# Performance work log

Measured on AMD Instinct MI355X. Metric: run time of the kernel, lower is better.

Reference implementation:

```python
import jax, jax.numpy as jnp
import numpy as np
from jax import lax

VOCAB, EMB, HID = 32000, 512, 1024
T, B = 256, 16


def setup_inputs() -> dict:
    key = jax.random.key(0)
    k1, k2, k3, k4, k5, k6 = jax.random.split(key, 6)
    s = lambda fan_in: 1.0 / np.sqrt(fan_in)
    return {
        "x": jax.random.randint(k1, (T, B), 0, VOCAB),
        "h": jnp.zeros((B, HID), jnp.float32),
        "emb": jax.random.normal(k2, (VOCAB, EMB), jnp.float32),
        "Wz": jax.random.normal(k3, (HID, EMB + HID), jnp.float32) * s(EMB + HID),
        "Wr": jax.random.normal(k4, (HID, EMB + HID), jnp.float32) * s(EMB + HID),
        "W": jax.random.normal(k5, (HID, EMB + HID), jnp.float32) * s(EMB + HID),
        "Wd": jax.random.normal(k6, (VOCAB, HID), jnp.float32) * s(HID),
    }


def reference(x, h, emb, Wz, Wr, W, Wd):
    x_emb = emb[x]  # [T, B, EMB]

    def step(h_prev, xe):
        y = jnp.concatenate([h_prev, xe], axis=1)           # [B, HID+EMB]
        z = jax.nn.sigmoid(y @ Wz.T)                        # [B, HID]
        r = jax.nn.sigmoid(y @ Wr.T)                        # [B, HID]
        cand = jnp.tanh(jnp.concatenate([r * h_prev, xe], axis=1) @ W.T)
        h_new = (1.0 - z) * h_prev + z * cand
        return h_new, h_new

    _, all_h = lax.scan(step, h, x_emb)                     # [T, B, HID]
    all_y = jnp.einsum('tbh,vh->tbv', all_h, Wd)            # [T, B, VOCAB]
    return all_h, all_y
```

## Files before the change

kernel.cpp:

```cpp
#include <hip/hip_runtime.h>


using bf16x8 = __attribute__((ext_vector_type(8))) __bf16;
using f32x4  = __attribute__((ext_vector_type(4))) float;

#define GRUB 64
#define TOTB 256
#define NTILE 250
#define NGRP  32

__device__ __forceinline__ unsigned short f2bf(float f) {
  unsigned u = __builtin_bit_cast(unsigned, f);
  u += 0x7FFFu + ((u >> 16) & 1u);
  return (unsigned short)(u >> 16);
}

__device__ __forceinline__ f32x4 mfma16(bf16x8 a, bf16x8 b, f32x4 c) {
  return __builtin_amdgcn_mfma_f32_16x16x32_bf16(a, b, c, 0, 0, 0);
}

__device__ __forceinline__ void ust32(unsigned* p, unsigned v) {
  __hip_atomic_store(p, v, __ATOMIC_RELAXED, __HIP_MEMORY_SCOPE_AGENT);
}
__device__ __forceinline__ unsigned uld32(const unsigned* p) {
  return __hip_atomic_load(p, __ATOMIC_RELAXED, __HIP_MEMORY_SCOPE_AGENT);
}


__global__ void prep_w(const float* __restrict__ Wz, const float* __restrict__ Wr,
                       const float* __restrict__ Wm,
                       unsigned short* __restrict__ Whall,
                       unsigned short* __restrict__ Wxall) {
  int i = blockIdx.x * 256 + threadIdx.x;
  int g   = i / 393216;
  int rem = i % 393216;
  int j   = rem / 384;
  int k   = (rem % 384) * 4;
  const float* src = (g == 0) ? Wz : (g == 1) ? Wr : Wm;
  float4 v = *(const float4*)(src + (size_t)j * 1536 + k);
  ushort4 o;
  o.x = f2bf(v.x); o.y = f2bf(v.y); o.z = f2bf(v.z); o.w = f2bf(v.w);
  if (k < 1024)
    *(ushort4*)(Whall + ((size_t)(g * 1024 + j) * 1024 + k)) = o;
  else
    *(ushort4*)(Wxall + ((size_t)(g * 1024 + j) * 512 + (k - 1024))) = o;
}

__global__ void prep_wd(const float* __restrict__ Wd, unsigned short* __restrict__ Wdbf) {
  size_t i = (size_t)blockIdx.x * 256 + threadIdx.x;
  float4 v = *(const float4*)(Wd + i * 4);
  ushort4 o;
  o.x = f2bf(v.x); o.y = f2bf(v.y); o.z = f2bf(v.z); o.w = f2bf(v.w);
  *(ushort4*)(Wdbf + i * 4) = o;
}

__global__ void prep_xe(const int* __restrict__ x, const float* __restrict__ emb,
                        unsigned short* __restrict__ xebf) {
  int i  = blockIdx.x * 256 + threadIdx.x;
  int tb = i >> 7, k = (i & 127) * 4;
  int tok = x[tb];
  float4 v = *(const float4*)(emb + (size_t)tok * 512 + k);
  ushort4 o;
  o.x = f2bf(v.x); o.y = f2bf(v.y); o.z = f2bf(v.z); o.w = f2bf(v.w);
  *(ushort4*)(xebf + (size_t)tb * 512 + k) = o;
}

__global__ void prep_h(const float* __restrict__ h, unsigned short* __restrict__ hbf) {
  int i = blockIdx.x * 256 + threadIdx.x;
  hbf[i] = f2bf(h[i]);
}

__global__ __launch_bounds__(256) void gemm_bt(
    const unsigned short* __restrict__ A, const unsigned short* __restrict__ B,
    float* __restrict__ C, int M, int N, int K, int lda, int ldb, int ldc) {
  __shared__ uint4 As[128 * 5];
  __shared__ uint4 Bs[128 * 5];
  const int tid  = threadIdx.x;
  const int wid  = tid >> 6, lane = tid & 63;
  const int wr   = wid >> 1, wc = wid & 1;
  const int m0   = blockIdx.x * 128, n0 = blockIdx.y * 128;
  const int lr   = lane & 15, lk = lane >> 4;

  f32x4 acc[4][4] = {};
  const int nk = K >> 5;
  for (int kt = 0; kt < nk; ++kt) {
#pragma unroll
    for (int c = 0; c < 2; ++c) {
      int chunk = c * 256 + tid;
      int row = chunk >> 2, kc = chunk & 3;
      As[row * 5 + kc] = *(const uint4*)(A + (size_t)(m0 + row) * lda + kt * 32 + kc * 8);
      Bs[row * 5 + kc] = *(const uint4*)(B + (size_t)(n0 + row) * ldb + kt * 32 + kc * 8);
    }
    __syncthreads();
    bf16x8 af[4], bg[4];
#pragma unroll
    for (int i = 0; i < 4; ++i) {
      af[i] = __builtin_bit_cast(bf16x8, As[(wr * 64 + i * 16 + lr) * 5 + lk]);
      bg[i] = __builtin_bit_cast(bf16x8, Bs[(wc * 64 + i * 16 + lr) * 5 + lk]);
    }
#pragma unroll
    for (int i = 0; i < 4; ++i)
#pragma unroll
      for (int j = 0; j < 4; ++j)
        acc[i][j] = mfma16(af[i], bg[j], acc[i][j]);
    __syncthreads();
  }
#pragma unroll
  for (int i = 0; i < 4; ++i) {
    int mb = m0 + wr * 64 + i * 16 + lk * 4;
#pragma unroll
    for (int j = 0; j < 4; ++j) {
      int n = n0 + wc * 64 + j * 16 + lr;
#pragma unroll
      for (int q = 0; q < 4; ++q)
        C[(size_t)(mb + q) * ldc + n] = acc[i][j][q];
    }
  }
}


__device__ __forceinline__ void flag_bar(unsigned* flags, unsigned seq) {
  __syncthreads();
  if (threadIdx.x < 64) {
    if (threadIdx.x == 0)
      ust32(&flags[blockIdx.x * 32], seq);
    unsigned* f = &flags[threadIdx.x * 32];
    while (uld32(f) < seq) {}
  }
  __syncthreads();
}

__global__ __launch_bounds__(256, 1) void mega(
    const unsigned short* __restrict__ Whall, const float* __restrict__ Gx,
    const unsigned short* __restrict__ h0bf, const float* __restrict__ h0f,
    unsigned short* __restrict__ rhs, float* __restrict__ outh,
    unsigned short* __restrict__ allh,
    const unsigned short* __restrict__ Wdbf, float* __restrict__ outy,
    unsigned* __restrict__ flags) {
  __shared__ uint4 smem[6672];
  const int tid = threadIdx.x;
  const int bid = blockIdx.x;
  unsigned* stepp = flags + 2048;
  unsigned* ctrp  = flags + 2080;

  if (bid < GRUB) {
    uint4* Wl = smem;
    float (*red)[4][16][16] = (float (*)[4][16][16])(smem + 6144);
    const int lane = tid & 63, wq = tid >> 6;
    const int c0   = bid * 16;
    const int lr   = lane & 15, lk = lane >> 4;
    const int bKu  = wq * 32;

    for (int it = 0; it < 24; ++it) {
      int chunk = it * 256 + tid;
      int g = chunk >> 11, rem = chunk & 2047;
      int cl = rem >> 7, k8 = rem & 127;
      uint4 v = *(const uint4*)(Whall + ((size_t)(g * 1024 + c0 + cl) * 1024 + k8 * 8));
      Wl[(g * 16 + cl) * 128 + (k8 ^ (cl & 7))] = v;
    }

    const int b_  = tid >> 4, cl_ = tid & 15;
    const int cg  = c0 + cl_;
    float hp = h0f[b_ * 1024 + cg];
    float zv = 0.f;
    __syncthreads();

    for (int t = 0; t < 256; ++t) {
      const size_t tb = (size_t)t * 16 + b_;
      float gz = Gx[tb * 3072 + cg];
      float gr = Gx[tb * 3072 + 1024 + cg];
      float gc = Gx[tb * 3072 + 2048 + cg];

      const uint4* hp4 = (t == 0) ? (const uint4*)h0bf
                                  : (const uint4*)(allh + (size_t)(t - 1) * 16384);
      f32x4 az = {}, ar = {};
#pragma unroll
      for (int kk = 0; kk < 8; ++kk) {
        int ku = bKu + kk * 4 + lk;
        bf16x8 a  = __builtin_bit_cast(bf16x8, hp4[lr * 128 + ku]);
        bf16x8 bz = __builtin_bit_cast(bf16x8, Wl[(0 * 16 + lr) * 128 + (ku ^ (lr & 7))]);
        bf16x8 br = __builtin_bit_cast(bf16x8, Wl[(1 * 16 + lr) * 128 + (ku ^ (lr & 7))]);
        az = mfma16(a, bz, az);
        ar = mfma16(a, br, ar);
      }
#pragma unroll
      for (int q = 0; q < 4; ++q) {
        red[0][wq][lk * 4 + q][lr] = az[q];
        red[1][wq][lk * 4 + q][lr] = ar[q];
      }
      __syncthreads();
      {
        float sz = red[0][0][b_][cl_] + red[0][1][b_][cl_] + red[0][2][b_][cl_] +
                   red[0][3][b_][cl_] + gz;
        float sr = red[1][0][b_][cl_] + red[1][1][b_][cl_] + red[1][2][b_][cl_] +
                   red[1][3][b_][cl_] + gr;
        zv = 1.f / (1.f + __expf(-sz));
        float rv = 1.f / (1.f + __expf(-sr));
        unsigned short my = f2bf(rv * hp);
        unsigned other = __shfl_xor((unsigned)my, 1);
        if ((cl_ & 1) == 0)
          ust32((unsigned*)rhs + (((size_t)t * 16384 + b_ * 1024 + cg) >> 1),
                (unsigned)my | (other << 16));
      }
      flag_bar(flags, 2 * t + 1);

      const uint4* rt4 = (const uint4*)(rhs + (size_t)t * 16384);
      f32x4 ac = {};
#pragma unroll
      for (int kk = 0; kk < 8; ++kk) {
        int ku = bKu + kk * 4 + lk;
        bf16x8 a  = __builtin_bit_cast(bf16x8, rt4[lr * 128 + ku]);
        bf16x8 bc = __builtin_bit_cast(bf16x8, Wl[(2 * 16 + lr) * 128 + (ku ^ (lr & 7))]);
        ac = mfma16(a, bc, ac);
      }
#pragma unroll
      for (int q = 0; q < 4; ++q) red[0][wq][lk * 4 + q][lr] = ac[q];
      __syncthreads();
      {
        float sc = red[0][0][b_][cl_] + red[0][1][b_][cl_] + red[0][2][b_][cl_] +
                   red[0][3][b_][cl_] + gc;
        float cand = tanhf(sc);
        float hn = (1.f - zv) * hp + zv * cand;
        hp = hn;
        outh[tb * 1024 + cg] = hn;
        unsigned short my = f2bf(hn);
        unsigned other = __shfl_xor((unsigned)my, 1);
        if ((cl_ & 1) == 0)
          ust32((unsigned*)allh + (((size_t)t * 16384 + b_ * 1024 + cg) >> 1),
                (unsigned)my | (other << 16));
      }
      flag_bar(flags, 2 * t + 2);
      if (bid == 0 && tid == 0) ust32(stepp, t + 1);
    }
  }

  __syncthreads();
  uint4* As = smem;
  uint4* Bs = smem + 640;
  unsigned* wsh = (unsigned*)(smem + 6656);
  const int wid = tid >> 6, lane = tid & 63;
  const int wr = wid >> 1, wc = wid & 1;
  const int lr = lane & 15, lk = lane >> 4;

  for (;;) {
    __syncthreads();
    if (tid == 0) {
      unsigned w = __hip_atomic_fetch_add(ctrp, 1u, __ATOMIC_RELAXED,
                                          __HIP_MEMORY_SCOPE_AGENT);
      if (w < (unsigned)(NGRP * NTILE)) {
        unsigned need = (w / NTILE) * 8u + 8u;
        while (uld32(stepp) < need) __builtin_amdgcn_s_sleep(32);
      }
      *wsh = w;
    }
    __syncthreads();
    unsigned w = *wsh;
    if (w >= (unsigned)(NGRP * NTILE)) break;
    int g = w / NTILE, nt = w % NTILE;
    int m0 = g * 128, n0 = nt * 128;

    f32x4 acc[4][4] = {};
    for (int kt = 0; kt < 32; ++kt) {
#pragma unroll
      for (int c = 0; c < 2; ++c) {
        int chunk = c * 256 + tid;
        int row = chunk >> 2, kc = chunk & 3;
        As[row * 5 + kc] = *(const uint4*)(allh + (size_t)(m0 + row) * 1024 + kt * 32 + kc * 8);
        Bs[row * 5 + kc] = *(const uint4*)(Wdbf + (size_t)(n0 + row) * 1024 + kt * 32 + kc * 8);
      }
      __syncthreads();
      bf16x8 af[4], bg[4];
#pragma unroll
      for (int i = 0; i < 4; ++i) {
        af[i] = __builtin_bit_cast(bf16x8, As[(wr * 64 + i * 16 + lr) * 5 + lk]);
        bg[i] = __builtin_bit_cast(bf16x8, Bs[(wc * 64 + i * 16 + lr) * 5 + lk]);
      }
#pragma unroll
      for (int i = 0; i < 4; ++i)
#pragma unroll
        for (int j = 0; j < 4; ++j)
          acc[i][j] = mfma16(af[i], bg[j], acc[i][j]);
      __syncthreads();
    }
#pragma unroll
    for (int i = 0; i < 4; ++i) {
      int mb = m0 + wr * 64 + i * 16 + lk * 4;
#pragma unroll
      for (int j = 0; j < 4; ++j) {
        int n = n0 + wc * 64 + j * 16 + lr;
#pragma unroll
        for (int q = 0; q < 4; ++q)
          outy[(size_t)(mb + q) * 32000 + n] = acc[i][j][q];
      }
    }
  }
}

constexpr size_t OFF_WH  = 0;
constexpr size_t OFF_WX  = OFF_WH + 3ull * 1024 * 1024 * 2;
constexpr size_t OFF_WD  = OFF_WX + 3ull * 1024 * 512 * 2;
constexpr size_t OFF_XE  = OFF_WD + 32000ull * 1024 * 2;
constexpr size_t OFF_GX  = OFF_XE + 4096ull * 512 * 2;
constexpr size_t OFF_AH  = OFF_GX + 4096ull * 3072 * 4;
constexpr size_t OFF_H0  = OFF_AH + 4096ull * 1024 * 2;
constexpr size_t OFF_RHS = OFF_H0 + 16384ull * 2;
constexpr size_t OFF_FLG = OFF_RHS + 256ull * 16384 * 2;

extern "C" void kernel_launch(void* const* d_in, const int* in_sizes, int n_in,
                              void* d_out, int out_size, void* d_ws, size_t ws_size,
                              hipStream_t stream) {
  const int*   x   = (const int*)d_in[0];
  const float* h0  = (const float*)d_in[1];
  const float* emb = (const float*)d_in[2];
  const float* Wz  = (const float*)d_in[3];
  const float* Wr  = (const float*)d_in[4];
  const float* Wm  = (const float*)d_in[5];
  const float* Wd  = (const float*)d_in[6];

  float* out_h = (float*)d_out;
  float* out_y = out_h + 4096ull * 1024;

  char* ws = (char*)d_ws;
  unsigned short* Whall = (unsigned short*)(ws + OFF_WH);
  unsigned short* Wxall = (unsigned short*)(ws + OFF_WX);
  unsigned short* Wdbf  = (unsigned short*)(ws + OFF_WD);
  unsigned short* xebf  = (unsigned short*)(ws + OFF_XE);
  float*          Gx    = (float*)(ws + OFF_GX);
  unsigned short* allh  = (unsigned short*)(ws + OFF_AH);
  unsigned short* h0bf  = (unsigned short*)(ws + OFF_H0);
  unsigned short* rhs   = (unsigned short*)(ws + OFF_RHS);
  unsigned*       flags = (unsigned*)(ws + OFF_FLG);

  hipMemsetAsync(flags, 0, 16384, stream);

  prep_w <<<4608, 256, 0, stream>>>(Wz, Wr, Wm, Whall, Wxall);
  prep_wd<<<32000, 256, 0, stream>>>(Wd, Wdbf);
  prep_xe<<<2048, 256, 0, stream>>>(x, emb, xebf);
  prep_h <<<64, 256, 0, stream>>>(h0, h0bf);

  gemm_bt<<<dim3(32, 24), 256, 0, stream>>>(xebf, Wxall, Gx,
                                            4096, 3072, 512, 512, 512, 3072);

  mega<<<TOTB, 256, 0, stream>>>(Whall, Gx, h0bf, h0, rhs,
                                 out_h, allh, Wdbf, out_y, flags);
}
```

Before: 1.486 ms.

## Replace block barriers with per-wave flags and fold Wd conversion into mega kernel

Swaps the grid-wide flag barrier (which needed two __syncthreads per phase) for per-wavefront flags, where each wave polls the 64 lanes of its own wave index. The step counter is dropped, and projection tiles now wait directly on the recurrence flags. The separate prep_wd launch is removed: the Wd-to-bf16 conversion runs as work items inside the persistent mega kernel on the idle blocks while the recurrence proceeds, so it overlaps. This adds memory-ordering subtlety, since it relies on s_waitcnt plus relaxed atomics, and it adds spin polling.

```diff
diff --git a/kernel.cpp b/kernel.cpp
--- a/kernel.cpp
+++ b/kernel.cpp
@@ -4,10 +4,12 @@
 using bf16x8 = __attribute__((ext_vector_type(8))) __bf16;
 using f32x4  = __attribute__((ext_vector_type(4))) float;
 
-#define GRUB 64
-#define TOTB 256
+#define GRUB  64
+#define TOTB  256
 #define NTILE 250
 #define NGRP  32
+#define NCONV 500
+#define NITEM (NCONV + NGRP * NTILE)
 
 __device__ __forceinline__ unsigned short f2bf(float f) {
   unsigned u = __builtin_bit_cast(unsigned, f);
@@ -22,9 +24,13 @@
 __device__ __forceinline__ void ust32(unsigned* p, unsigned v) {
   __hip_atomic_store(p, v, __ATOMIC_RELAXED, __HIP_MEMORY_SCOPE_AGENT);
 }
+__device__ __forceinline__ void ust64(unsigned long long* p, unsigned long long v) {
+  __hip_atomic_store(p, v, __ATOMIC_RELAXED, __HIP_MEMORY_SCOPE_AGENT);
+}
 __device__ __forceinline__ unsigned uld32(const unsigned* p) {
   return __hip_atomic_load(p, __ATOMIC_RELAXED, __HIP_MEMORY_SCOPE_AGENT);
 }
+__device__ __forceinline__ unsigned umin_(unsigned a, unsigned b) { return a < b ? a : b; }
 
 
 __global__ void prep_w(const float* __restrict__ Wz, const float* __restrict__ Wr,
@@ -46,14 +52,6 @@
     *(ushort4*)(Wxall + ((size_t)(g * 1024 + j) * 512 + (k - 1024))) = o;
 }
 
-__global__ void prep_wd(const float* __restrict__ Wd, unsigned short* __restrict__ Wdbf) {
-  size_t i = (size_t)blockIdx.x * 256 + threadIdx.x;
-  float4 v = *(const float4*)(Wd + i * 4);
-  ushort4 o;
-  o.x = f2bf(v.x); o.y = f2bf(v.y); o.z = f2bf(v.z); o.w = f2bf(v.w);
-  *(ushort4*)(Wdbf + i * 4) = o;
-}
-
 __global__ void prep_xe(const int* __restrict__ x, const float* __restrict__ emb,
                         unsigned short* __restrict__ xebf) {
   int i  = blockIdx.x * 256 + threadIdx.x;
@@ -119,29 +117,18 @@
 }
 
 
-__device__ __forceinline__ void flag_bar(unsigned* flags, unsigned seq) {
-  __syncthreads();
-  if (threadIdx.x < 64) {
-    if (threadIdx.x == 0)
-      ust32(&flags[blockIdx.x * 32], seq);
-    unsigned* f = &flags[threadIdx.x * 32];
-    while (uld32(f) < seq) {}
-  }
-  __syncthreads();
-}
-
 __global__ __launch_bounds__(256, 1) void mega(
     const unsigned short* __restrict__ Whall, const float* __restrict__ Gx,
     const unsigned short* __restrict__ h0bf, const float* __restrict__ h0f,
     unsigned short* __restrict__ rhs, float* __restrict__ outh,
     unsigned short* __restrict__ allh,
-    const unsigned short* __restrict__ Wdbf, float* __restrict__ outy,
-    unsigned* __restrict__ flags) {
-  __shared__ uint4 smem[6672];
+    const float* __restrict__ Wd, unsigned short* __restrict__ Wdbf,
+    float* __restrict__ outy, unsigned* __restrict__ flags) {
+  __shared__ uint4 smem[6928];
   const int tid = threadIdx.x;
   const int bid = blockIdx.x;
-  unsigned* stepp = flags + 2048;
-  unsigned* ctrp  = flags + 2080;
+  unsigned* ctrp  = flags + 512;
+  unsigned* convp = flags + 544;
 
   if (bid < GRUB) {
     uint4* Wl = smem;
@@ -161,6 +148,8 @@
 
     const int b_  = tid >> 4, cl_ = tid & 15;
     const int cg  = c0 + cl_;
+    unsigned* myflag = flags + (bid << 2) + wq;
+    const unsigned* pollf = flags + (wq << 6) + lane;
     float hp = h0f[b_ * 1024 + cg];
     float zv = 0.f;
     __syncthreads();
@@ -170,6 +159,11 @@
       float gz = Gx[tb * 3072 + cg];
       float gr = Gx[tb * 3072 + 1024 + cg];
       float gc = Gx[tb * 3072 + 2048 + cg];
+
+      if (t > 0) {
+        while (uld32(pollf) < 2u * (unsigned)t) {}
+      }
+      asm volatile("" ::: "memory");
 
       const uint4* hp4 = (t == 0) ? (const uint4*)h0bf
                                   : (const uint4*)(allh + (size_t)(t - 1) * 16384);
@@ -202,7 +196,11 @@
           ust32((unsigned*)rhs + (((size_t)t * 16384 + b_ * 1024 + cg) >> 1),
                 (unsigned)my | (other << 16));
       }
-      flag_bar(flags, 2 * t + 1);
+      asm volatile("s_waitcnt vmcnt(0)" ::: "memory");
+      if (lane == 0) ust32(myflag, 2u * (unsigned)t + 1u);
+
+      while (uld32(pollf) < 2u * (unsigned)t + 1u) {}
+      asm volatile("" ::: "memory");
 
       const uint4* rt4 = (const uint4*)(rhs + (size_t)t * 16384);
       f32x4 ac = {};
@@ -214,50 +212,79 @@
         ac = mfma16(a, bc, ac);
       }
 #pragma unroll
-      for (int q = 0; q < 4; ++q) red[0][wq][lk * 4 + q][lr] = ac[q];
-      __syncthreads();
+      for (int q = 0; q < 4; ++q) red[2][wq][lk * 4 + q][lr] = ac[q];
+      __syncthreads();
+      float hn;
       {
-        float sc = red[0][0][b_][cl_] + red[0][1][b_][cl_] + red[0][2][b_][cl_] +
-                   red[0][3][b_][cl_] + gc;
+        float sc = red[2][0][b_][cl_] + red[2][1][b_][cl_] + red[2][2][b_][cl_] +
+                   red[2][3][b_][cl_] + gc;
         float cand = tanhf(sc);
-        float hn = (1.f - zv) * hp + zv * cand;
+        hn = (1.f - zv) * hp + zv * cand;
         hp = hn;
-        outh[tb * 1024 + cg] = hn;
         unsigned short my = f2bf(hn);
         unsigned other = __shfl_xor((unsigned)my, 1);
         if ((cl_ & 1) == 0)
           ust32((unsigned*)allh + (((size_t)t * 16384 + b_ * 1024 + cg) >> 1),
                 (unsigned)my | (other << 16));
       }
-      flag_bar(flags, 2 * t + 2);
-      if (bid == 0 && tid == 0) ust32(stepp, t + 1);
+      asm volatile("s_waitcnt vmcnt(0)" ::: "memory");
+      if (lane == 0) ust32(myflag, 2u * (unsigned)t + 2u);
+      outh[tb * 1024 + cg] = hn;
     }
   }
 
   __syncthreads();
   uint4* As = smem;
   uint4* Bs = smem + 640;
-  unsigned* wsh = (unsigned*)(smem + 6656);
+  unsigned* wsh = (unsigned*)(smem + 6920);
   const int wid = tid >> 6, lane = tid & 63;
   const int wr = wid >> 1, wc = wid & 1;
   const int lr = lane & 15, lk = lane >> 4;
 
   for (;;) {
     __syncthreads();
-    if (tid == 0) {
-      unsigned w = __hip_atomic_fetch_add(ctrp, 1u, __ATOMIC_RELAXED,
-                                          __HIP_MEMORY_SCOPE_AGENT);
-      if (w < (unsigned)(NGRP * NTILE)) {
-        unsigned need = (w / NTILE) * 8u + 8u;
-        while (uld32(stepp) < need) __builtin_amdgcn_s_sleep(32);
-      }
-      *wsh = w;
-    }
+    if (tid == 0)
+      *wsh = __hip_atomic_fetch_add(ctrp, 1u, __ATOMIC_RELAXED,
+                                    __HIP_MEMORY_SCOPE_AGENT);
     __syncthreads();
     unsigned w = *wsh;
-    if (w >= (unsigned)(NGRP * NTILE)) break;
-    int g = w / NTILE, nt = w % NTILE;
+    if (w >= (unsigned)NITEM) break;
+
+    if (w < (unsigned)NCONV) {
+      const float4* src = (const float4*)Wd + (size_t)w * 16384;
+      unsigned long long* dst = (unsigned long long*)Wdbf + (size_t)w * 16384;
+      for (int it = 0; it < 64; ++it) {
+        int idx = it * 256 + tid;
+        float4 v = src[idx];
+        ushort4 o;
+        o.x = f2bf(v.x); o.y = f2bf(v.y); o.z = f2bf(v.z); o.w = f2bf(v.w);
+        ust64(dst + idx, __builtin_bit_cast(unsigned long long, o));
+      }
+      asm volatile("s_waitcnt vmcnt(0)" ::: "memory");
+      __syncthreads();
+      if (tid == 0)
+        __hip_atomic_fetch_add(convp, 1u, __ATOMIC_RELAXED,
+                               __HIP_MEMORY_SCOPE_AGENT);
+      continue;
+    }
+
+    unsigned p = w - NCONV;
+    int g = p / NTILE, nt = p % NTILE;
     int m0 = g * 128, n0 = nt * 128;
+
+    unsigned tgt = 16u * (unsigned)g + 16u;
+    if (tid < 64) {
+      const unsigned* f = flags + tid * 4;
+      for (;;) {
+        unsigned mn = umin_(umin_(uld32(f), uld32(f + 1)),
+                            umin_(uld32(f + 2), uld32(f + 3)));
+        if (mn >= tgt) break;
+        __builtin_amdgcn_s_sleep(8);
+      }
+    }
+    if (tid == 0)
+      while (uld32(convp) < (unsigned)NCONV) __builtin_amdgcn_s_sleep(8);
+    __syncthreads();
 
     f32x4 acc[4][4] = {};
     for (int kt = 0; kt < 32; ++kt) {
@@ -334,7 +361,6 @@
   hipMemsetAsync(flags, 0, 16384, stream);
 
   prep_w <<<4608, 256, 0, stream>>>(Wz, Wr, Wm, Whall, Wxall);
-  prep_wd<<<32000, 256, 0, stream>>>(Wd, Wdbf);
   prep_xe<<<2048, 256, 0, stream>>>(x, emb, xebf);
   prep_h <<<64, 256, 0, stream>>>(h0, h0bf);
 
@@ -342,5 +368,5 @@
                                             4096, 3072, 512, 512, 512, 3072);
 
   mega<<<TOTB, 256, 0, stream>>>(Whall, Gx, h0bf, h0, rhs,
-                                 out_h, allh, Wdbf, out_y, flags);
-}
+                                 out_h, allh, Wd, Wdbf, out_y, flags);
+}
```

Measured after the change: 2.918 ms. +96.3%, slower.
